# Kernel tuning notes

Measured on AMD Instinct MI355X. Metric: run time of the kernel, lower is better.

Reference implementation:

```python
import jax, jax.numpy as jnp
import numpy as np

G1, G2, G3 = 4.0, 5.0, 10.0   # cfg.SMOOTH.GAMMA1/2/3 (DAMSM defaults)
T_MOCO = 0.05
EPS = 1e-8


def _ce(logits, labels):
    # mean cross-entropy, labels are int class indices
    lp = jax.nn.log_softmax(logits, axis=-1)
    return -jnp.mean(jnp.take_along_axis(lp, labels[:, None], axis=1)[:, 0])


def _norm(x):
    return jnp.sqrt(jnp.sum(x * x, axis=-1, keepdims=True))


def setup_inputs() -> dict:
    key = jax.random.key(0)
    ks = jax.random.split(key, 8)
    B, T, NEF, H, K = 64, 32, 256, 17, 16384
    return {
        "cnn_code": jax.random.normal(ks[0], (B, NEF), jnp.float32),
        "rnn_code": jax.random.normal(ks[1], (B, NEF), jnp.float32),
        "img_features": jax.random.normal(ks[2], (B, NEF, H, H), jnp.float32),
        "words_emb": jax.random.normal(ks[3], (B, T, NEF), jnp.float32),
        "cnn_code_aug": jax.random.normal(ks[4], (B, NEF), jnp.float32),
        "rnn_code_aug": jax.random.normal(ks[5], (B, NEF), jnp.float32),
        "queue": jax.random.normal(ks[6], (NEF, K), jnp.float32),
        "queue_im": jax.random.normal(ks[7], (NEF, K), jnp.float32),
        "sentence_mask": jnp.ones((B, T), jnp.int32),
        "labels": jnp.arange(B, dtype=jnp.int32),
    }


def reference(cnn_code, rnn_code, img_features, words_emb, cnn_code_aug,
              rnn_code_aug, queue, queue_im, sentence_mask, labels):
    B = words_emb.shape[0]
    # ---------- local word-region attention loss (vectorized over the
    # per-sample python loop; sentence_mask is all-ones -> full length) ----------
    q = jnp.transpose(words_emb, (0, 2, 1))                   # [B, nef, T]
    ctx = img_features.reshape(B, img_features.shape[1], -1)  # [B, nef, S]
    # func_attention: scores[i,j,s,t] between query sample i and image j
    scores = jnp.einsum('jcs,ict->ijst', ctx, q)
    attn = jax.nn.softmax(scores, axis=3)        # softmax over words (queryL)
    attn = jax.nn.softmax(G1 * attn, axis=2)     # softmax over regions (sourceL)
    wC = jnp.einsum('jcs,ijst->ijct', ctx, attn)  # weighted context [i,j,nef,T]
    num = jnp.einsum('ict,ijct->ijt', q, wC)
    qn = jnp.sqrt(jnp.sum(q * q, axis=1))[:, None, :]         # [B,1,T]
    wn = jnp.sqrt(jnp.sum(wC * wC, axis=2))                   # [B,B,T]
    cos = num / jnp.clip(qn * wn, EPS, None)                  # [i,j,T]
    sim = jax.nn.logsumexp(G2 * cos, axis=2)                  # log(sum exp(G2*cos))
    S = sim.T * G3                                            # [j, i] as in original cat(dim=1)
    w_loss0 = _ce(S, labels)
    w_loss1 = _ce(S.T, labels)
    # ---------- global contrastive loss ----------
    cn = cnn_code / jnp.clip(_norm(cnn_code), EPS, None)
    rn = rnn_code / jnp.clip(_norm(rnn_code), EPS, None)
    can = cnn_code_aug / jnp.clip(_norm(cnn_code_aug), EPS, None)
    ran = rnn_code_aug / jnp.clip(_norm(rnn_code_aug), EPS, None)
    qz = jax.lax.stop_gradient(queue)
    qzi = jax.lax.stop_gradient(queue_im)
    zeros = jnp.zeros((B,), dtype=labels.dtype)
    log_it = jnp.concatenate([jnp.sum(cn * ran, -1, keepdims=True), cn @ qz], -1) / T_MOCO
    log_ti = jnp.concatenate([jnp.sum(rn * can, -1, keepdims=True), rn @ qzi], -1) / T_MOCO
    m_loss = (_ce(log_it, zeros) + _ce(log_ti, zeros)) / 2.0
    s0 = G3 * (cn @ rn.T)    # cosine(cnn, rnn) * GAMMA3
    s2 = G3 * (rn @ ran.T)   # cosine(rnn, rnn_aug) * GAMMA3
    loss0 = _ce(s0, labels)
    loss1 = _ce(s0.T, labels)
    loss2 = _ce(s2, labels)
    loss3 = _ce(s2.T, labels)
    return jnp.stack([w_loss0, w_loss1, loss0, loss1, m_loss, loss2, loss3])
```

## Files before the change

kernel.cpp:

```cpp
#include <hip/hip_runtime.h>
#include <hip/hip_bf16.h>
#include <math.h>

#define BB   64
#define TT   32
#define CC   256
#define KK   16384
#define G1c  4.0f
#define G2c  5.0f
#define G3c  10.0f
#define INV_T 20.0f
#define EPSF 1e-8f

#define WS_SIM 0
#define WS_S0  4096
#define WS_S2  8192
#define WS_CN  12288
#define WS_RN  28672
#define WS_CAN 45056
#define WS_RAN 61440
#define WS_QN  77824
#define WS_PM  79872
#define WS_PS  (WS_PM + 16384)
#define WS_CNT  (WS_PS + 16384)
#define WS_RNT  (WS_CNT + 16384)
#define WS_CANT (WS_RNT + 16384)
#define WS_RANT (WS_CANT + 16384)
#define WS_F32_TOTAL (WS_RANT + 16384)

#define CTXT_ELEMS (64*320*256)
#define CTXC_ELEMS (64*256*320)
#define WQ_ELEMS   (64*32*256)
#define CNRN_OFF   (CTXT_ELEMS + CTXC_ELEMS + WQ_ELEMS)

#define SC_STR 260

typedef __attribute__((ext_vector_type(8))) short short8;
typedef __attribute__((ext_vector_type(4))) short short4v;
typedef __attribute__((ext_vector_type(4))) float float4v;

__device__ __forceinline__ float4v mfma_bf16(short8 a, short8 b, float4v c) {
    return __builtin_amdgcn_mfma_f32_16x16x32_bf16(a, b, c, 0, 0, 0);
}

__device__ __forceinline__ short f2bf(float f) {
    union { float f; unsigned u; } x; x.f = f;
    unsigned r = x.u + 0x7FFFu + ((x.u >> 16) & 1u);
    return (short)(r >> 16);
}

__device__ __forceinline__ short8 ld8(const short* p) {
    short4v lo = *(const short4v*)p;
    short4v hi = *(const short4v*)(p + 4);
    short8 r = {lo[0],lo[1],lo[2],lo[3],hi[0],hi[1],hi[2],hi[3]};
    return r;
}

__global__ __launch_bounds__(256) void prep_kernel(
    const float* __restrict__ cnn, const float* __restrict__ rnn,
    const float* __restrict__ img, const float* __restrict__ wemb,
    const float* __restrict__ cnnA, const float* __restrict__ rnnA,
    float* __restrict__ W)
{
    int bid = blockIdx.x, tid = threadIdx.x;
    short* B16 = (short*)(W + WS_F32_TOTAL);
    short* ctxT = B16;
    short* ctxC = B16 + CTXT_ELEMS;
    short* wq   = B16 + CTXT_ELEMS + CTXC_ELEMS;
    short* cnrn = B16 + CNRN_OFF;

    if (bid < 256) {
        int mat = bid >> 6, row = bid & 63;
        const float* src = (mat==0)? cnn : (mat==1)? rnn : (mat==2)? cnnA : rnnA;
        float* dst  = W + ((mat==0)? WS_CN  : (mat==1)? WS_RN  : (mat==2)? WS_CAN  : WS_RAN);
        float* dstT = W + ((mat==0)? WS_CNT : (mat==1)? WS_RNT : (mat==2)? WS_CANT : WS_RANT);
        float v = src[row*256 + tid];
        float ss = v*v;
        for (int o=1;o<64;o<<=1) ss += __shfl_xor(ss,o);
        __shared__ float sc[4];
        if ((tid&63)==0) sc[tid>>6] = ss;
        __syncthreads();
        float tot = sc[0]+sc[1]+sc[2]+sc[3];
        float inv = 1.0f / fmaxf(sqrtf(tot), EPSF);
        float nv = v*inv;
        dst[row*256+tid] = nv;
        dstT[tid*64+row] = nv;
        if (mat < 2) cnrn[(mat*64+row)*256 + tid] = f2bf(nv);
    } else if (bid < 320) {
        int i = bid - 256;
        int t = tid >> 3, k = tid & 7;
        const float* wp = wemb + (i*32 + t)*256 + k*32;
        float ss = 0.f;
        for (int c=0;c<32;c++){ float v = wp[c]; ss += v*v; }
        ss += __shfl_xor(ss,1); ss += __shfl_xor(ss,2); ss += __shfl_xor(ss,4);
        if (k==0) W[WS_QN + i*32 + t] = sqrtf(ss);
    } else if (bid < 1600) {
        int b3 = bid - 320; int j = b3 / 20, mt = b3 % 20, s0 = mt*16;
        __shared__ float tile[16*257];
        for (int idx = tid; idx < 4096; idx += 256) {
            int c = idx >> 4, sl = idx & 15, s = s0 + sl;
            float v = (s < 289) ? img[((size_t)(j*256 + c))*289 + s] : 0.0f;
            tile[sl*257 + c] = v;
        }
        __syncthreads();
        for (int idx = tid; idx < 4096; idx += 256) {
            int orr = idx >> 8, c = idx & 255;
            ctxT[((size_t)(j*320 + s0 + orr))*256 + c] = f2bf(tile[orr*257 + c]);
        }
        {
            int c = tid;
            short tmp[16];
            #pragma unroll
            for (int sl = 0; sl < 16; sl++) tmp[sl] = f2bf(tile[sl*257 + c]);
            short* dstc = ctxC + ((size_t)(j*256 + c))*320 + s0;
            #pragma unroll
            for (int k2 = 0; k2 < 4; k2++) {
                short4v w = { tmp[k2*4], tmp[k2*4+1], tmp[k2*4+2], tmp[k2*4+3] };
                *(short4v*)(dstc + k2*4) = w;
            }
        }
    } else {
        for (int idx = (bid-1600)*256 + tid; idx < WQ_ELEMS; idx += 64*256) {
            wq[idx] = f2bf(wemb[idx]);
        }
    }
}

__global__ __launch_bounds__(256, 2) void attn_moco_kernel(
    const float* __restrict__ queue, const float* __restrict__ queueIm,
    float* __restrict__ W)
{
    __shared__ short ctx_sc[32*SC_STR];
    __shared__ short eTile[2][2][32][36];
    __shared__ float Dp[4][32], Np[4][32];
    __shared__ float wn2P[4][2][2][16];
    __shared__ float redm[4][64], reds[4][64];
    __shared__ float sa0[256], sa1[256];
    __shared__ float part[2][64][4];

    int bid = blockIdx.x, tid = threadIdx.x;
    int lane = tid & 63, wave = tid >> 6;
    int lo16 = lane & 15, quad = lane >> 4;

    const short* B16 = (const short*)(W + WS_F32_TOTAL);

    if (bid < 2048) {
        const short* ctxT = B16;
        const short* ctxC = B16 + CTXT_ELEMS;
        const short* wq   = B16 + CTXT_ELEMS + CTXC_ELEMS;

        int j = bid >> 5, ip = bid & 31;
        int i_l = wave >> 1, mt = wave & 1;
        int i_g = ip*2 + i_l;

        short8 bq[2][8];
        {
            const short* p = wq + i_g*8192;
            #pragma unroll
            for (int nt2=0;nt2<2;nt2++)
                #pragma unroll
                for (int kk=0;kk<8;kk++)
                    bq[nt2][kk] = *(const short8*)(p + (nt2*16+lo16)*256 + kk*32 + quad*8);
        }

        float4v wacc[4][4];
        #pragma unroll
        for (int cm=0;cm<4;cm++)
            #pragma unroll
            for (int cb=0;cb<4;cb++) wacc[cm][cb] = (float4v){0.f,0.f,0.f,0.f};
        float D0=0.f, D1=0.f, N0=0.f, N1=0.f;

        const short* ctxTj = ctxT + (size_t)j * (320*256);
        const short* ctxCj = ctxC + (size_t)j * (256*320);
        int s_row = tid >> 3, c0s = (tid & 7)*32;
        int srow_base = mt*16 + quad*4;

        short8 pf[4];
        {
            const short* g = ctxTj + s_row*256 + c0s;
            #pragma unroll
            for (int m=0;m<4;m++) pf[m] = *(const short8*)(g + m*8);
        }

        for (int tile = 0; tile < 10; tile++) {
            {
                short* d = ctx_sc + s_row*SC_STR + c0s;
                #pragma unroll
                for (int k=0;k<8;k++) {
                    short4v w = { pf[k>>1][(k&1)*4+0], pf[k>>1][(k&1)*4+1],
                                  pf[k>>1][(k&1)*4+2], pf[k>>1][(k&1)*4+3] };
                    *(short4v*)(d + k*4) = w;
                }
            }
            __syncthreads();
            if (tile < 9) {
                const short* g = ctxTj + ((tile+1)*32 + s_row)*256 + c0s;
                #pragma unroll
                for (int m=0;m<4;m++) pf[m] = *(const short8*)(g + m*8);
            }
            short8 wa[4];
            #pragma unroll
            for (int cm=0;cm<4;cm++)
                wa[cm] = *(const short8*)(ctxCj + (size_t)((wave*4+cm)*16+lo16)*320 + tile*32 + quad*8);

            float4v a0 = {0.f,0.f,0.f,0.f}, a1 = {0.f,0.f,0.f,0.f};
            {
                const short* ar = ctx_sc + (mt*16 + lo16)*SC_STR + quad*8;
                #pragma unroll
                for (int kk=0;kk<8;kk++) {
                    short8 a = ld8(ar + kk*32);
                    a0 = mfma_bf16(a, bq[0][kk], a0);
                    a1 = mfma_bf16(a, bq[1][kk], a1);
                }
            }
            int eb = tile & 1;
            #pragma unroll
            for (int r=0;r<4;r++) {
                float mx = fmaxf(a0[r], a1[r]);
                mx = fmaxf(mx, __shfl_xor(mx,1));
                mx = fmaxf(mx, __shfl_xor(mx,2));
                mx = fmaxf(mx, __shfl_xor(mx,4));
                mx = fmaxf(mx, __shfl_xor(mx,8));
                float e0 = __expf(a0[r]-mx), e1 = __expf(a1[r]-mx);
                float z = e0 + e1;
                z += __shfl_xor(z,1); z += __shfl_xor(z,2);
                z += __shfl_xor(z,4); z += __shfl_xor(z,8);
                float rinv = 1.0f/z;
                int s_local = srow_base + r;
                int sg = tile*32 + s_local;
                float ev0 = 0.f, ev1 = 0.f;
                if (sg < 289) {
                    ev0 = __expf(G1c*e0*rinv);
                    ev1 = __expf(G1c*e1*rinv);
                    D0 += ev0; N0 += ev0*a0[r];
                    D1 += ev1; N1 += ev1*a1[r];
                }
                eTile[eb][i_l][lo16][s_local]    = f2bf(ev0);
                eTile[eb][i_l][16+lo16][s_local] = f2bf(ev1);
            }
            __syncthreads();
            {
                short8 bf0 = ld8(&eTile[eb][0][lo16][quad*8]);
                short8 bf1 = ld8(&eTile[eb][0][16+lo16][quad*8]);
                short8 bf2 = ld8(&eTile[eb][1][lo16][quad*8]);
                short8 bf3 = ld8(&eTile[eb][1][16+lo16][quad*8]);
                #pragma unroll
                for (int cm=0;cm<4;cm++) {
                    wacc[cm][0] = mfma_bf16(wa[cm], bf0, wacc[cm][0]);
                    wacc[cm][1] = mfma_bf16(wa[cm], bf1, wacc[cm][1]);
                    wacc[cm][2] = mfma_bf16(wa[cm], bf2, wacc[cm][2]);
                    wacc[cm][3] = mfma_bf16(wa[cm], bf3, wacc[cm][3]);
                }
            }
        }

        D0 += __shfl_xor(D0,16); D0 += __shfl_xor(D0,32);
        D1 += __shfl_xor(D1,16); D1 += __shfl_xor(D1,32);
        N0 += __shfl_xor(N0,16); N0 += __shfl_xor(N0,32);
        N1 += __shfl_xor(N1,16); N1 += __shfl_xor(N1,32);
        if (lane < 16) {
            Dp[wave][lane] = D0; Dp[wave][16+lane] = D1;
            Np[wave][lane] = N0; Np[wave][16+lane] = N1;
        }
        #pragma unroll
        for (int cb=0;cb<4;cb++) {
            float ss = 0.f;
            #pragma unroll
            for (int cm=0;cm<4;cm++)
                #pragma unroll
                for (int r=0;r<4;r++){ float v = wacc[cm][cb][r]; ss += v*v; }
            ss += __shfl_xor(ss,16);
            ss += __shfl_xor(ss,32);
            if (quad==0) wn2P[wave][cb>>1][cb&1][lo16] = ss;
        }
        __syncthreads();

        if (tid < 64) {
            int i_f = tid >> 5, t = tid & 31;
            int nt2 = t >> 4, lo = t & 15;
            float w2 = wn2P[0][i_f][nt2][lo] + wn2P[1][i_f][nt2][lo]
                     + wn2P[2][i_f][nt2][lo] + wn2P[3][i_f][nt2][lo];
            float D = Dp[i_f*2][t] + Dp[i_f*2+1][t];
            float N = Np[i_f*2][t] + Np[i_f*2+1][t];
            int i_gf = ip*2 + i_f;
            float qv = W[WS_QN + i_gf*32 + t];
            float numS = N/D;
            float wnS = sqrtf(w2)/D;
            float v = G2c * (numS / fmaxf(qv*wnS, EPSF));
            float mx = v;
            for (int o=1;o<32;o<<=1) mx = fmaxf(mx, __shfl_xor(mx,o));
            float e = __expf(v-mx);
            for (int o=1;o<32;o<<=1) e += __shfl_xor(e,o);
            if (t==0) W[WS_SIM + i_gf*64 + j] = mx + __logf(e);
        }
    } else if (bid < 2304) {
        int bid2 = bid - 2048;
        int mu = bid2 >> 7, ch = bid2 & 127;
        const float* Q = mu ? queueIm : queue;
        const short* Abf = B16 + CNRN_OFF + mu*16384;

        short8 afr[4][8];
        #pragma unroll
        for (int mt=0;mt<4;mt++)
            #pragma unroll
            for (int kk=0;kk<8;kk++)
                afr[mt][kk] = *(const short8*)(Abf + (mt*16+lo16)*256 + kk*32 + quad*8);

        float m16[16], s16[16];
        #pragma unroll
        for (int u=0;u<16;u++){ m16[u] = -1e30f; s16[u] = 0.f; }

        for (int t4 = 0; t4 < 2; t4++) {
            int colb = ch*128 + (wave*2 + t4)*16;
            float4v acc[4];
            #pragma unroll
            for (int mt=0;mt<4;mt++) acc[mt] = (float4v){0.f,0.f,0.f,0.f};
            for (int ks = 0; ks < 8; ks++) {
                short8 bfr;
                #pragma unroll
                for (int jj=0;jj<8;jj++) {
                    float bv = Q[(size_t)(ks*32 + quad*8 + jj)*KK + colb + lo16];
                    bfr[jj] = f2bf(bv);
                }
                #pragma unroll
                for (int mt=0;mt<4;mt++) acc[mt] = mfma_bf16(afr[mt][ks], bfr, acc[mt]);
            }
            #pragma unroll
            for (int mt=0;mt<4;mt++)
                #pragma unroll
                for (int r=0;r<4;r++) {
                    float v = acc[mt][r]*INV_T;
                    int u = mt*4+r;
                    float nm = fmaxf(m16[u], v);
                    s16[u] = s16[u]*__expf(m16[u]-nm) + __expf(v-nm);
                    m16[u] = nm;
                }
        }
        #pragma unroll
        for (int u=0;u<16;u++) {
            #pragma unroll
            for (int o=1;o<16;o<<=1) {
                float om = __shfl_xor(m16[u],o), os = __shfl_xor(s16[u],o);
                float nm = fmaxf(m16[u],om);
                s16[u] = s16[u]*__expf(m16[u]-nm) + os*__expf(om-nm);
                m16[u] = nm;
            }
        }
        if (lo16 == 0) {
            #pragma unroll
            for (int u=0;u<16;u++) {
                int row = (u>>2)*16 + quad*4 + (u&3);
                redm[wave][row] = m16[u]; reds[wave][row] = s16[u];
            }
        }
        __syncthreads();
        if (tid < 64) {
            float m = redm[0][tid], s = reds[0][tid];
            for (int w=1;w<4;w++) {
                float om = redm[w][tid], os = reds[w][tid];
                float nm = fmaxf(m,om);
                s = s*__expf(m-nm) + os*__expf(om-nm);
                m = nm;
            }
            W[WS_PM + mu*8192 + ch*64 + tid] = m;
            W[WS_PS + mu*8192 + ch*64 + tid] = s;
        }
    } else {
        int i = bid - 2304;
        sa0[tid] = W[WS_CN + i*256 + tid];
        sa1[tid] = W[WS_RN + i*256 + tid];
        __syncthreads();
        const float* B0 = W + WS_RN;
        const float* B1v = W + WS_RAN;
        float av0 = sa0[tid], av1 = sa1[tid];
        for (int jj = 0; jj < 64; jj++) {
            float v0 = av0 * B0[jj*256 + tid];
            float v1 = av1 * B1v[jj*256 + tid];
            for (int o=1;o<64;o<<=1){ v0 += __shfl_xor(v0,o); v1 += __shfl_xor(v1,o); }
            if (lane==0){ part[0][jj][wave]=v0; part[1][jj][wave]=v1; }
        }
        __syncthreads();
        if (tid < 128) {
            int mat = tid>>6, jj = tid&63;
            float s = part[mat][jj][0]+part[mat][jj][1]+part[mat][jj][2]+part[mat][jj][3];
            W[(mat? WS_S2 : WS_S0) + i*64 + jj] = G3c * s;
        }
    }
}

__global__ __launch_bounds__(256) void final_kernel(
    const int* __restrict__ labels, float* __restrict__ W, float* __restrict__ out)
{
    int tid = threadIdx.x;
    __shared__ float mats[3][64][65];
    __shared__ float mmL[2][4][64], ssL[2][4][64];
    __shared__ float cearr[6][64];
    __shared__ float cemoco[128];

    for (int idx = tid; idx < 3*4096; idx += 256) {
        int t = idx >> 12, rem = idx & 4095;
        const float* src = W + (t==0 ? WS_SIM : (t==1 ? WS_S0 : WS_S2));
        mats[t][rem>>6][rem&63] = src[rem];
    }

    {
        int g = tid >> 6, r = tid & 63;
        for (int mu=0; mu<2; mu++) {
            float m = -1e30f, s = 0.f;
            for (int k=0; k<32; k++) {
                int ch = g*32 + k;
                float om = W[WS_PM + mu*8192 + ch*64 + r];
                float os = W[WS_PS + mu*8192 + ch*64 + r];
                float nm = fmaxf(m, om);
                s = s*__expf(m-nm) + os*__expf(om-nm);
                m = nm;
            }
            mmL[mu][g][r] = m; ssL[mu][g][r] = s;
        }
    }
    __syncthreads();

    if (tid < 128) {
        int mu = tid>>6, r = tid&63;
        float m = mmL[mu][0][r], s = ssL[mu][0][r];
        for (int g=1; g<4; g++) {
            float om = mmL[mu][g][r], os = ssL[mu][g][r];
            float nm = fmaxf(m, om);
            s = s*__expf(m-nm) + os*__expf(om-nm);
            m = nm;
        }
        const float* AT = W + (mu ? WS_RNT : WS_CNT);
        const float* BT = W + (mu ? WS_CANT : WS_RANT);
        float dot = 0.f;
        for (int c=0; c<256; c++) dot += AT[c*64 + r]*BT[c*64 + r];
        float v0 = dot*INV_T;
        float nm = fmaxf(m, v0);
        float S = s*__expf(m-nm) + __expf(v0-nm);
        cemoco[tid] = nm + __logf(S) - v0;
    }

    for (int pass=0; pass<2; pass++) {
        int cfg = pass*4 + (tid>>6);
        int row = tid&63;
        if (cfg < 6) {
            int mi; float scale; int colMajor;
            if (cfg==0){ mi=0; scale=G3c; colMajor=1; }
            else if (cfg==1){ mi=0; scale=G3c; colMajor=0; }
            else if (cfg==2){ mi=1; scale=1.f; colMajor=0; }
            else if (cfg==3){ mi=1; scale=1.f; colMajor=1; }
            else if (cfg==4){ mi=2; scale=1.f; colMajor=0; }
            else            { mi=2; scale=1.f; colMajor=1; }
            float mx = -1e30f;
            for (int x=0;x<64;x++) {
                float v = (colMajor? mats[mi][x][row] : mats[mi][row][x])*scale;
                mx = fmaxf(mx, v);
            }
            float se = 0.f;
            for (int x=0;x<64;x++) {
                float v = (colMajor? mats[mi][x][row] : mats[mi][row][x])*scale;
                se += __expf(v-mx);
            }
            int lbl = labels[row];
            float diag = (colMajor? mats[mi][lbl][row] : mats[mi][row][lbl])*scale;
            cearr[cfg][row] = mx + __logf(se) - diag;
        }
    }
    __syncthreads();

    if (tid < 7) {
        float r;
        if (tid == 4) {
            float s0=0.f, s1=0.f;
            for (int k=0;k<64;k++){ s0 += cemoco[k]; s1 += cemoco[64+k]; }
            r = (s0/64.f + s1/64.f)*0.5f;
        } else {
            int cfg = (tid < 4) ? tid : tid - 1;
            float s = 0.f;
            for (int k=0;k<64;k++) s += cearr[cfg][k];
            r = s/64.f;
        }
        out[tid] = r;
    }
}

extern "C" void kernel_launch(void* const* d_in, const int* in_sizes, int n_in,
                              void* d_out, int out_size, void* d_ws, size_t ws_size,
                              hipStream_t stream)
{
    const float* cnn   = (const float*)d_in[0];
    const float* rnn   = (const float*)d_in[1];
    const float* img   = (const float*)d_in[2];
    const float* wemb  = (const float*)d_in[3];
    const float* cnnA  = (const float*)d_in[4];
    const float* rnnA  = (const float*)d_in[5];
    const float* queue   = (const float*)d_in[6];
    const float* queueIm = (const float*)d_in[7];
    const int*   labels  = (const int*)d_in[9];
    float* W   = (float*)d_ws;
    float* out = (float*)d_out;

    prep_kernel<<<1664, 256, 0, stream>>>(cnn, rnn, img, wemb, cnnA, rnnA, W);
    attn_moco_kernel<<<2368, 256, 0, stream>>>(queue, queueIm, W);
    final_kernel<<<1, 256, 0, stream>>>(labels, W, out);
}
```

Baseline: 272.5 us.

## Drop channel-major ctx copy; read transposed fragments from LDS and reorder blocks

Removes the second bf16 copy of the image context (channel-major layout) written by the prep kernel. The attention kernel now builds the weighted-context MFMA operands by strided reads from the already-staged shared-memory tile instead of separate global loads. The short MoCo and global blocks are moved to the front of the grid so they get scheduled first. This saves prep-kernel writes and global read traffic, at the cost of 8 scalar, likely bank-conflicted LDS reads per fragment.

```diff
diff --git a/kernel.cpp b/kernel.cpp
--- a/kernel.cpp
+++ b/kernel.cpp
@@ -29,9 +29,9 @@
 #define WS_F32_TOTAL (WS_RANT + 16384)
 
 #define CTXT_ELEMS (64*320*256)
-#define CTXC_ELEMS (64*256*320)
 #define WQ_ELEMS   (64*32*256)
-#define CNRN_OFF   (CTXT_ELEMS + CTXC_ELEMS + WQ_ELEMS)
+#define WQ_OFF     CTXT_ELEMS
+#define CNRN_OFF   (CTXT_ELEMS + WQ_ELEMS)
 
 #define SC_STR 260
 
@@ -65,8 +65,7 @@
     int bid = blockIdx.x, tid = threadIdx.x;
     short* B16 = (short*)(W + WS_F32_TOTAL);
     short* ctxT = B16;
-    short* ctxC = B16 + CTXT_ELEMS;
-    short* wq   = B16 + CTXT_ELEMS + CTXC_ELEMS;
+    short* wq   = B16 + WQ_OFF;
     short* cnrn = B16 + CNRN_OFF;
 
     if (bid < 256) {
@@ -107,18 +106,6 @@
             int orr = idx >> 8, c = idx & 255;
             ctxT[((size_t)(j*320 + s0 + orr))*256 + c] = f2bf(tile[orr*257 + c]);
         }
-        {
-            int c = tid;
-            short tmp[16];
-            #pragma unroll
-            for (int sl = 0; sl < 16; sl++) tmp[sl] = f2bf(tile[sl*257 + c]);
-            short* dstc = ctxC + ((size_t)(j*256 + c))*320 + s0;
-            #pragma unroll
-            for (int k2 = 0; k2 < 4; k2++) {
-                short4v w = { tmp[k2*4], tmp[k2*4+1], tmp[k2*4+2], tmp[k2*4+3] };
-                *(short4v*)(dstc + k2*4) = w;
-            }
-        }
     } else {
         for (int idx = (bid-1600)*256 + tid; idx < WQ_ELEMS; idx += 64*256) {
             wq[idx] = f2bf(wemb[idx]);
@@ -144,12 +131,12 @@
 
     const short* B16 = (const short*)(W + WS_F32_TOTAL);
 
-    if (bid < 2048) {
+    if (bid >= 320) {
         const short* ctxT = B16;
-        const short* ctxC = B16 + CTXT_ELEMS;
-        const short* wq   = B16 + CTXT_ELEMS + CTXC_ELEMS;
-
-        int j = bid >> 5, ip = bid & 31;
+        const short* wq   = B16 + WQ_OFF;
+
+        int abid = bid - 320;
+        int j = abid >> 5, ip = abid & 31;
         int i_l = wave >> 1, mt = wave & 1;
         int i_g = ip*2 + i_l;
 
@@ -171,7 +158,6 @@
         float D0=0.f, D1=0.f, N0=0.f, N1=0.f;
 
         const short* ctxTj = ctxT + (size_t)j * (320*256);
-        const short* ctxCj = ctxC + (size_t)j * (256*320);
         int s_row = tid >> 3, c0s = (tid & 7)*32;
         int srow_base = mt*16 + quad*4;
 
@@ -198,10 +184,6 @@
                 #pragma unroll
                 for (int m=0;m<4;m++) pf[m] = *(const short8*)(g + m*8);
             }
-            short8 wa[4];
-            #pragma unroll
-            for (int cm=0;cm<4;cm++)
-                wa[cm] = *(const short8*)(ctxCj + (size_t)((wave*4+cm)*16+lo16)*320 + tile*32 + quad*8);
 
             float4v a0 = {0.f,0.f,0.f,0.f}, a1 = {0.f,0.f,0.f,0.f};
             {
@@ -213,6 +195,17 @@
                     a1 = mfma_bf16(a, bq[1][kk], a1);
                 }
             }
+
+            short8 wa[4];
+            #pragma unroll
+            for (int cm=0;cm<4;cm++) {
+                const short* col = ctx_sc + quad*8*SC_STR + wave*64 + cm*16 + lo16;
+                short8 v;
+                #pragma unroll
+                for (int jj=0;jj<8;jj++) v[jj] = col[jj*SC_STR];
+                wa[cm] = v;
+            }
+
             int eb = tile & 1;
             #pragma unroll
             for (int r=0;r<4;r++) {
@@ -293,9 +286,8 @@
             for (int o=1;o<32;o<<=1) e += __shfl_xor(e,o);
             if (t==0) W[WS_SIM + i_gf*64 + j] = mx + __logf(e);
         }
-    } else if (bid < 2304) {
-        int bid2 = bid - 2048;
-        int mu = bid2 >> 7, ch = bid2 & 127;
+    } else if (bid < 256) {
+        int mu = bid >> 7, ch = bid & 127;
         const float* Q = mu ? queueIm : queue;
         const short* Abf = B16 + CNRN_OFF + mu*16384;
 
@@ -366,7 +358,7 @@
             W[WS_PS + mu*8192 + ch*64 + tid] = s;
         }
     } else {
-        int i = bid - 2304;
+        int i = bid - 256;
         sa0[tid] = W[WS_CN + i*256 + tid];
         sa1[tid] = W[WS_RN + i*256 + tid];
         __syncthreads();
```

After: 251.8 us. -7.6%, faster.
